# Kernel tuning notes

Measured on AMD Instinct MI355X. Metric: run time of the kernel, lower is better.

The kernel has to match this reference:

```python
import jax, jax.numpy as jnp
import numpy as np

DIM = 1024
HEADS = 16
N_SENTS = 64
N_ENTS = 16
BATCH = 32


def setup_inputs() -> dict:
    key = jax.random.key(0)
    ks = jax.random.split(key, 16)
    S, E, B, D = N_SENTS, N_ENTS, BATCH, DIM
    sc = 1.0 / np.sqrt(D)
    f32 = jnp.float32
    return {
        "entities": jax.random.normal(ks[0], (S * E, B, D), f32),
        "padding_mask": jnp.zeros((S * E, B), bool),
        "n_sents": S,
        # learned aggregation query, init uniform(-1, 1) as in the module
        "query": jax.random.uniform(ks[1], (1, 1, D), f32, -1.0, 1.0),
        # do_proj key/val Linear layers (torch Linear convention: y = x @ W.T + b)
        "Wk_lin": jax.random.normal(ks[2], (D, D), f32) * sc,
        "bk_lin": jnp.zeros((D,), f32),
        "Wv_lin": jax.random.normal(ks[3], (D, D), f32) * sc,
        "bv_lin": jnp.zeros((D,), f32),
        # MultiheadAttention in-projection (split q/k/v) and out-projection
        "Wq_in": jax.random.normal(ks[4], (D, D), f32) * sc,
        "bq_in": jnp.zeros((D,), f32),
        "Wk_in": jax.random.normal(ks[5], (D, D), f32) * sc,
        "bk_in": jnp.zeros((D,), f32),
        "Wv_in": jax.random.normal(ks[6], (D, D), f32) * sc,
        "bv_in": jnp.zeros((D,), f32),
        "Wo": jax.random.normal(ks[7], (D, D), f32) * sc,
        "bo": jnp.zeros((D,), f32),
    }


def reference(entities, padding_mask, n_sents, query,
              Wk_lin, bk_lin, Wv_lin, bv_lin,
              Wq_in, bq_in, Wk_in, bk_in, Wv_in, bv_in, Wo, bo):
    SE, B, D = entities.shape
    E = SE // n_sents
    H = HEADS
    hd = D // H

    # do_proj key/value linears
    keys = entities @ Wk_lin.T + bk_lin   # [SE, B, D]
    vals = entities @ Wv_lin.T + bv_lin   # [SE, B, D]

    # MHA in-projections. Query is a single learned vector shared across
    # sentences and batch, so project once: [H, hd], pre-scaled by 1/sqrt(hd).
    q = ((query[0, 0] @ Wq_in.T + bq_in).reshape(H, hd)) * (1.0 / np.sqrt(hd))
    # Honor the block-diagonal mask: query s only sees its n_ents key slice,
    # so reshape keys/vals to [S, E, B, H, hd] and never build [S, S*E] scores.
    k = (keys @ Wk_in.T + bk_in).reshape(n_sents, E, B, H, hd)
    v = (vals @ Wv_in.T + bv_in).reshape(n_sents, E, B, H, hd)

    scores = jnp.einsum('hd,sebhd->sbhe', q, k)            # [S, B, H, E]
    pm = padding_mask.reshape(n_sents, E, B).transpose(0, 2, 1)  # [S, B, E]
    scores = jnp.where(pm[:, :, None, :], -jnp.inf, scores)
    attn = jax.nn.softmax(scores, axis=-1)                 # [S, B, H, E]
    ctx = jnp.einsum('sbhe,sebhd->sbhd', attn, v).reshape(n_sents, B, D)
    return ctx @ Wo.T + bo                                  # [S, B, D]
```

## Files before the change

kernel.cpp:

```cpp
#include <hip/hip_runtime.h>
#include <hip/hip_bf16.h>

constexpr int kD  = 1024;
constexpr int kH  = 16;
constexpr int kHD = 64;
constexpr int kS  = 64;
constexpr int kE  = 16;
constexpr int kB  = 32;
constexpr int kSB = kS * kB;

typedef __attribute__((ext_vector_type(8))) short bfvec8;
typedef __attribute__((ext_vector_type(4))) float fvec4;

struct __align__(8)  bf4  { __hip_bfloat16 v[4]; };
struct __align__(16) bf8v { __hip_bfloat16 v[8]; };


__global__ __launch_bounds__(256) void k_rowdot(const float* __restrict__ Wmat,
                                                const float* __restrict__ vec,
                                                const float* __restrict__ bias,
                                                float scale, float* __restrict__ outv) {
  int j = blockIdx.x;
  int t = threadIdx.x;
  const float4* w4 = (const float4*)(Wmat + (size_t)j * kD);
  const float4* v4 = (const float4*)vec;
  float4 a = w4[t], b = v4[t];
  float acc = a.x * b.x + a.y * b.y + a.z * b.z + a.w * b.w;
  #pragma unroll
  for (int o = 32; o >= 1; o >>= 1) acc += __shfl_xor(acc, o);
  __shared__ float red[4];
  if ((t & 63) == 0) red[t >> 6] = acc;
  __syncthreads();
  if (t == 0) outv[j] = (red[0] + red[1] + red[2] + red[3] + bias[j]) * scale;
}

__global__ __launch_bounds__(256) void k_w(const float* __restrict__ qs,
                                           const float* __restrict__ Wk_in,
                                           float* __restrict__ wmat) {
  int tid = blockIdx.x * 256 + threadIdx.x;
  int h = tid >> 10, d = tid & (kD - 1);
  float acc = 0.f;
  #pragma unroll 8
  for (int j = 0; j < kHD; j++)
    acc = fmaf(qs[h * kHD + j], Wk_in[(size_t)(h * kHD + j) * kD + d], acc);
  wmat[(size_t)h * kD + d] = acc;
}

__global__ __launch_bounds__(256) void k_c(const float* __restrict__ wmat,
                                           const float* __restrict__ bk_lin,
                                           const float* __restrict__ qs,
                                           const float* __restrict__ bk_in,
                                           float* __restrict__ cvec) {
  int t = threadIdx.x;
  int h = t >> 4, l = t & 15;
  float acc = 0.f;
  for (int d = l; d < kD; d += 16) acc += wmat[h * kD + d] * bk_lin[d];
  for (int j = l; j < kHD; j += 16) acc += qs[h * kHD + j] * bk_in[h * kHD + j];
  #pragma unroll
  for (int o = 8; o >= 1; o >>= 1) acc += __shfl_xor(acc, o, 16);
  if (l == 0) cvec[h] = acc;
}

__global__ void k_transpose_cvt(const float* __restrict__ in,
                                __hip_bfloat16* __restrict__ out) {
  __shared__ float tile[32][33];
  int x = blockIdx.x * 32 + threadIdx.x;
  int y0 = blockIdx.y * 32;
  for (int i = threadIdx.y; i < 32; i += 8)
    tile[i][threadIdx.x] = in[(size_t)(y0 + i) * kD + x];
  __syncthreads();
  int xo = blockIdx.y * 32 + threadIdx.x;
  int yo0 = blockIdx.x * 32;
  for (int i = threadIdx.y; i < 32; i += 8)
    out[(size_t)(yo0 + i) * kD + xo] = __float2bfloat16(tile[threadIdx.x][i]);
}


__global__ __launch_bounds__(256) void k_attn_eagg(const float* __restrict__ ent,
                                                   const unsigned char* __restrict__ pmask,
                                                   const __hip_bfloat16* __restrict__ Ubf,
                                                   const float* __restrict__ cvec,
                                                   __hip_bfloat16* __restrict__ eagg) {
  __shared__ __hip_bfloat16 ent_s[kE][kD + 8];
  __shared__ float sred[4][kE][kH + 1];
  __shared__ __hip_bfloat16 attn_b[kH][32];
  int sb = blockIdx.x;
  int s = sb >> 5, b = sb & 31;
  int t = threadIdx.x, l = t & 63, w = t >> 6;
  int quad = l >> 4, lane16 = l & 15;

  const float* src = ent + (size_t)(s * kE) * kB * kD + (size_t)b * kD;
  #pragma unroll
  for (int it = 0; it < 8; it++) {
    int i = t + it * 256;
    int e = i >> 7, f = (i & 127) * 8;
    const float4* pp = (const float4*)(src + (size_t)e * kB * kD + f);
    float4 v0 = pp[0], v1 = pp[1];
    bf8v pk;
    pk.v[0] = __float2bfloat16(v0.x); pk.v[1] = __float2bfloat16(v0.y);
    pk.v[2] = __float2bfloat16(v0.z); pk.v[3] = __float2bfloat16(v0.w);
    pk.v[4] = __float2bfloat16(v1.x); pk.v[5] = __float2bfloat16(v1.y);
    pk.v[6] = __float2bfloat16(v1.z); pk.v[7] = __float2bfloat16(v1.w);
    *(bf8v*)&ent_s[e][f] = pk;
  }
  __syncthreads();

  fvec4 sacc = {};
  #pragma unroll
  for (int ks = 0; ks < 8; ks++) {
    int k0 = w * 256 + ks * 32 + quad * 8;
    bfvec8 a = *(const bfvec8*)&ent_s[lane16][k0];
    bfvec8 bb = *(const bfvec8*)&Ubf[(size_t)lane16 * kD + k0];
    sacc = __builtin_amdgcn_mfma_f32_16x16x32_bf16(a, bb, sacc, 0, 0, 0);
  }
  #pragma unroll
  for (int i = 0; i < 4; i++) sred[w][quad * 4 + i][lane16] = sacc[i];
  __syncthreads();

  {
    int h = t >> 4, e = t & 15;
    float sc = sred[0][e][h] + sred[1][e][h] + sred[2][e][h] + sred[3][e][h] + cvec[h];
    if (pmask[(size_t)(s * kE + e) * kB + b]) sc = -INFINITY;
    float m = sc;
    #pragma unroll
    for (int o = 8; o >= 1; o >>= 1) m = fmaxf(m, __shfl_xor(m, o, 16));
    float ex = __expf(sc - m);
    float sum = ex;
    #pragma unroll
    for (int o = 8; o >= 1; o >>= 1) sum += __shfl_xor(sum, o, 16);
    attn_b[h][e] = __float2bfloat16(ex / sum);
    attn_b[h][e + 16] = __float2bfloat16(0.f);
  }
  __syncthreads();

  bfvec8 bfrag = *(const bfvec8*)&attn_b[lane16][quad * 8];
  __hip_bfloat16* dst = eagg + (size_t)sb * (kH * kD);
  for (int tt = 0; tt < 16; tt++) {
    int dme = (w * 16 + tt) * 16 + lane16;
    bfvec8 afrag = {};
    if (quad < 2) {
      #pragma unroll
      for (int j = 0; j < 8; j++)
        afrag[j] = *(const short*)&ent_s[quad * 8 + j][dme];
    }
    fvec4 acc = {};
    acc = __builtin_amdgcn_mfma_f32_16x16x32_bf16(afrag, bfrag, acc, 0, 0, 0);
    int d0 = (w * 16 + tt) * 16 + quad * 4;
    bf4 o;
    o.v[0] = __float2bfloat16(acc[0]); o.v[1] = __float2bfloat16(acc[1]);
    o.v[2] = __float2bfloat16(acc[2]); o.v[3] = __float2bfloat16(acc[3]);
    *(bf4*)&dst[(size_t)lane16 * kD + d0] = o;
  }
}


__device__ __forceinline__ void stage_row(const __hip_bfloat16* g, __hip_bfloat16* s) {
  *(bf8v*)s = *(const bf8v*)g;
}
__device__ __forceinline__ void stage_row(const float* g, __hip_bfloat16* s) {
  const float4* p = (const float4*)g;
  float4 v0 = p[0], v1 = p[1];
  bf8v pk;
  pk.v[0] = __float2bfloat16(v0.x); pk.v[1] = __float2bfloat16(v0.y);
  pk.v[2] = __float2bfloat16(v0.z); pk.v[3] = __float2bfloat16(v0.w);
  pk.v[4] = __float2bfloat16(v1.x); pk.v[5] = __float2bfloat16(v1.y);
  pk.v[6] = __float2bfloat16(v1.z); pk.v[7] = __float2bfloat16(v1.w);
  *(bf8v*)s = pk;
}

template <int MODE, typename TA, typename TB, typename TC>
__global__ __launch_bounds__(256) void k_gemm_mfma(
    const TA* __restrict__ Abase, int lda, long aBatch,
    const TB* __restrict__ Bbase, int ldb, long bBatch,
    TC* __restrict__ Cbase, int ldc, long cBatch,
    const float* __restrict__ bias, long biasBatch, int Ksz) {
  const TA* Ag = Abase + (size_t)blockIdx.z * aBatch;
  const TB* Bg = Bbase + (size_t)blockIdx.z * bBatch;
  TC* Cg = Cbase + (size_t)blockIdx.z * cBatch;
  const float* biasp = bias ? bias + (size_t)blockIdx.z * biasBatch : nullptr;
  const int m0 = blockIdx.x * 64, n0 = blockIdx.y * 64;
  __shared__ __hip_bfloat16 As[64][72];
  __shared__ __hip_bfloat16 Bs[64][72];
  const int t = threadIdx.x;
  const int l = t & 63, w = t >> 6;
  const int quad = l >> 4, col = l & 15;
  fvec4 acc[4] = {};
  for (int k0 = 0; k0 < Ksz; k0 += 64) {
    #pragma unroll
    for (int c = t; c < 512; c += 256) {
      int row = c >> 3, kq = (c & 7) * 8;
      stage_row(Ag + (size_t)(m0 + row) * lda + k0 + kq, &As[row][kq]);
      stage_row(Bg + (size_t)(n0 + row) * ldb + k0 + kq, &Bs[row][kq]);
    }
    __syncthreads();
    #pragma unroll
    for (int ks = 0; ks < 64; ks += 32) {
      bfvec8 a = *(const bfvec8*)&As[w * 16 + col][ks + quad * 8];
      #pragma unroll
      for (int nt = 0; nt < 4; nt++) {
        bfvec8 b = *(const bfvec8*)&Bs[nt * 16 + col][ks + quad * 8];
        acc[nt] = __builtin_amdgcn_mfma_f32_16x16x32_bf16(a, b, acc[nt], 0, 0, 0);
      }
    }
    __syncthreads();
  }
  #pragma unroll
  for (int nt = 0; nt < 4; nt++) {
    int n = n0 + nt * 16 + col;
    float bv = biasp ? biasp[n] : 0.f;
    #pragma unroll
    for (int i = 0; i < 4; i++) {
      int r = m0 + w * 16 + quad * 4 + i;
      float v = acc[nt][i] + bv;
      if constexpr (MODE == 0) {
        ((float*)Cg)[(size_t)r * ldc + n] = v;
      } else {
        ((__hip_bfloat16*)Cg)[(size_t)r * ldc + n] = __float2bfloat16(v);
      }
    }
  }
}

extern "C" void kernel_launch(void* const* d_in, const int* in_sizes, int n_in,
                              void* d_out, int out_size, void* d_ws, size_t ws_size,
                              hipStream_t stream) {
  const float* ent            = (const float*)d_in[0];
  const unsigned char* pmask  = (const unsigned char*)d_in[1];
  const float* query          = (const float*)d_in[3];
  const float* Wk_lin         = (const float*)d_in[4];
  const float* bk_lin         = (const float*)d_in[5];
  const float* Wv_lin         = (const float*)d_in[6];
  const float* bv_lin         = (const float*)d_in[7];
  const float* Wq_in          = (const float*)d_in[8];
  const float* bq_in          = (const float*)d_in[9];
  const float* Wk_in          = (const float*)d_in[10];
  const float* bk_in          = (const float*)d_in[11];
  const float* Wv_in          = (const float*)d_in[12];
  const float* bv_in          = (const float*)d_in[13];
  const float* Wo             = (const float*)d_in[14];
  const float* bo             = (const float*)d_in[15];
  float* out = (float*)d_out;

  float* p = (float*)d_ws;
  float* qs   = p; p += 1024;
  float* wmat = p; p += 64 * kD;
  float* cvec = p; p += 256;
  float* cb   = p; p += kD;
  __hip_bfloat16* bp = (__hip_bfloat16*)p;
  __hip_bfloat16* TT   = bp; bp += (size_t)kD * kD;
  __hip_bfloat16* Ubf  = bp; bp += (size_t)64 * kD;
  __hip_bfloat16* Mmat = bp; bp += (size_t)kD * kD;
  __hip_bfloat16* ctx2 = bp; bp += (size_t)kSB * kD;
  __hip_bfloat16* eagg = bp;

  k_rowdot<<<kD, 256, 0, stream>>>(Wq_in, query, bq_in, 0.125f, qs);
  k_w<<<64, 256, 0, stream>>>(qs, Wk_in, wmat);
  k_c<<<1, 256, 0, stream>>>(wmat, bk_lin, qs, bk_in, cvec);
  k_rowdot<<<kD, 256, 0, stream>>>(Wv_in, bv_lin, bv_in, 1.0f, cb);
  k_transpose_cvt<<<dim3(32, 32), dim3(32, 8), 0, stream>>>(Wk_lin, TT);
  k_gemm_mfma<2><<<dim3(1, 16, 1), 256, 0, stream>>>(
      wmat, kD, 0L, TT, kD, 0L, Ubf, kD, 0L, (const float*)nullptr, 0L, kD);
  k_transpose_cvt<<<dim3(32, 32), dim3(32, 8), 0, stream>>>(Wv_lin, TT);
  k_gemm_mfma<2><<<dim3(16, 16, 1), 256, 0, stream>>>(
      Wv_in, kD, 0L, TT, kD, 0L, Mmat, kD, 0L, (const float*)nullptr, 0L, kD);

  k_attn_eagg<<<kSB, 256, 0, stream>>>(ent, pmask, Ubf, cvec, eagg);
  k_gemm_mfma<2><<<dim3(kSB / 64, 1, kH), 256, 0, stream>>>(
      eagg, kH * kD, (long)kD, Mmat, kD, (long)(kHD * kD),
      ctx2, kD, (long)kHD, cb, (long)kHD, kD);
  k_gemm_mfma<0><<<dim3(kSB / 64, kD / 64, 1), 256, 0, stream>>>(
      ctx2, kD, 0L, Wo, kD, 0L, out, kD, 0L, bo, 0L, kD);
}
```

Baseline: 375.1 us.

## Use 128x64 GEMM tiles, pre-convert Wo to bf16, stage eagg stores via LDS

Adds a GEMM variant where each wave computes a 32x64 tile, so the block covers 128x64. Each B fragment is reused across two A fragments, and three GEMMs switch to it. Wo is converted to bf16 once up front instead of being restaged from fp32 in every tile. The attention kernel writes its aggregated output to shared memory first, then stores it to global memory in coalesced 16-byte chunks. In exchange, the bigger tiles halve the grid size on some GEMMs and LDS use rises in the attention kernel, which may lower occupancy.

```diff
diff --git a/kernel.cpp b/kernel.cpp
--- a/kernel.cpp
+++ b/kernel.cpp
@@ -75,6 +75,16 @@
     out[(size_t)(yo0 + i) * kD + xo] = __float2bfloat16(tile[threadIdx.x][i]);
 }
 
+__global__ __launch_bounds__(256) void k_cvt(const float* __restrict__ in,
+                                             __hip_bfloat16* __restrict__ out) {
+  int i = (blockIdx.x * 256 + threadIdx.x) * 4;
+  float4 v = *(const float4*)(in + i);
+  bf4 o;
+  o.v[0] = __float2bfloat16(v.x); o.v[1] = __float2bfloat16(v.y);
+  o.v[2] = __float2bfloat16(v.z); o.v[3] = __float2bfloat16(v.w);
+  *(bf4*)(out + i) = o;
+}
+
 
 __global__ __launch_bounds__(256) void k_attn_eagg(const float* __restrict__ ent,
                                                    const unsigned char* __restrict__ pmask,
@@ -82,6 +92,7 @@
                                                    const float* __restrict__ cvec,
                                                    __hip_bfloat16* __restrict__ eagg) {
   __shared__ __hip_bfloat16 ent_s[kE][kD + 8];
+  __shared__ __hip_bfloat16 eagg_s[kH][kD + 8];
   __shared__ float sred[4][kE][kH + 1];
   __shared__ __hip_bfloat16 attn_b[kH][32];
   int sb = blockIdx.x;
@@ -134,7 +145,6 @@
   __syncthreads();
 
   bfvec8 bfrag = *(const bfvec8*)&attn_b[lane16][quad * 8];
-  __hip_bfloat16* dst = eagg + (size_t)sb * (kH * kD);
   for (int tt = 0; tt < 16; tt++) {
     int dme = (w * 16 + tt) * 16 + lane16;
     bfvec8 afrag = {};
@@ -149,7 +159,16 @@
     bf4 o;
     o.v[0] = __float2bfloat16(acc[0]); o.v[1] = __float2bfloat16(acc[1]);
     o.v[2] = __float2bfloat16(acc[2]); o.v[3] = __float2bfloat16(acc[3]);
-    *(bf4*)&dst[(size_t)lane16 * kD + d0] = o;
+    *(bf4*)&eagg_s[lane16][d0] = o;
+  }
+  __syncthreads();
+
+  __hip_bfloat16* dstg = eagg + (size_t)sb * (kH * kD);
+  #pragma unroll
+  for (int it = 0; it < 8; it++) {
+    int c = t + it * 256;
+    int h = c >> 7, dq = (c & 127) * 8;
+    *(bf8v*)(dstg + (size_t)h * kD + dq) = *(const bf8v*)&eagg_s[h][dq];
   }
 }
 
@@ -212,10 +231,67 @@
     for (int i = 0; i < 4; i++) {
       int r = m0 + w * 16 + quad * 4 + i;
       float v = acc[nt][i] + bv;
-      if constexpr (MODE == 0) {
-        ((float*)Cg)[(size_t)r * ldc + n] = v;
-      } else {
-        ((__hip_bfloat16*)Cg)[(size_t)r * ldc + n] = __float2bfloat16(v);
+      if constexpr (MODE == 0) ((float*)Cg)[(size_t)r * ldc + n] = v;
+      else ((__hip_bfloat16*)Cg)[(size_t)r * ldc + n] = __float2bfloat16(v);
+    }
+  }
+}
+
+
+template <int MODE, typename TA, typename TB, typename TC>
+__global__ __launch_bounds__(256) void k_gemm_mfma2(
+    const TA* __restrict__ Abase, int lda, long aBatch,
+    const TB* __restrict__ Bbase, int ldb, long bBatch,
+    TC* __restrict__ Cbase, int ldc, long cBatch,
+    const float* __restrict__ bias, long biasBatch, int Ksz) {
+  const TA* Ag = Abase + (size_t)blockIdx.z * aBatch;
+  const TB* Bg = Bbase + (size_t)blockIdx.z * bBatch;
+  TC* Cg = Cbase + (size_t)blockIdx.z * cBatch;
+  const float* biasp = bias ? bias + (size_t)blockIdx.z * biasBatch : nullptr;
+  const int m0 = blockIdx.x * 128, n0 = blockIdx.y * 64;
+  __shared__ __hip_bfloat16 As[128][72];
+  __shared__ __hip_bfloat16 Bs[64][72];
+  const int t = threadIdx.x;
+  const int l = t & 63, w = t >> 6;
+  const int quad = l >> 4, col = l & 15;
+  fvec4 acc[2][4] = {};
+  for (int k0 = 0; k0 < Ksz; k0 += 64) {
+    #pragma unroll
+    for (int c = t; c < 1024; c += 256) {
+      int row = c >> 3, kq = (c & 7) * 8;
+      stage_row(Ag + (size_t)(m0 + row) * lda + k0 + kq, &As[row][kq]);
+    }
+    #pragma unroll
+    for (int c = t; c < 512; c += 256) {
+      int row = c >> 3, kq = (c & 7) * 8;
+      stage_row(Bg + (size_t)(n0 + row) * ldb + k0 + kq, &Bs[row][kq]);
+    }
+    __syncthreads();
+    #pragma unroll
+    for (int ks = 0; ks < 64; ks += 32) {
+      bfvec8 a0 = *(const bfvec8*)&As[w * 32 + col][ks + quad * 8];
+      bfvec8 a1 = *(const bfvec8*)&As[w * 32 + 16 + col][ks + quad * 8];
+      #pragma unroll
+      for (int nt = 0; nt < 4; nt++) {
+        bfvec8 b = *(const bfvec8*)&Bs[nt * 16 + col][ks + quad * 8];
+        acc[0][nt] = __builtin_amdgcn_mfma_f32_16x16x32_bf16(a0, b, acc[0][nt], 0, 0, 0);
+        acc[1][nt] = __builtin_amdgcn_mfma_f32_16x16x32_bf16(a1, b, acc[1][nt], 0, 0, 0);
+      }
+    }
+    __syncthreads();
+  }
+  #pragma unroll
+  for (int nt = 0; nt < 4; nt++) {
+    int n = n0 + nt * 16 + col;
+    float bv = biasp ? biasp[n] : 0.f;
+    #pragma unroll
+    for (int mi = 0; mi < 2; mi++) {
+      #pragma unroll
+      for (int i = 0; i < 4; i++) {
+        int r = m0 + w * 32 + mi * 16 + quad * 4 + i;
+        float v = acc[mi][nt][i] + bv;
+        if constexpr (MODE == 0) ((float*)Cg)[(size_t)r * ldc + n] = v;
+        else ((__hip_bfloat16*)Cg)[(size_t)r * ldc + n] = __float2bfloat16(v);
       }
     }
   }
@@ -250,9 +326,11 @@
   __hip_bfloat16* TT   = bp; bp += (size_t)kD * kD;
   __hip_bfloat16* Ubf  = bp; bp += (size_t)64 * kD;
   __hip_bfloat16* Mmat = bp; bp += (size_t)kD * kD;
+  __hip_bfloat16* Wobf = bp; bp += (size_t)kD * kD;
   __hip_bfloat16* ctx2 = bp; bp += (size_t)kSB * kD;
   __hip_bfloat16* eagg = bp;
 
+  k_cvt<<<kD, 256, 0, stream>>>(Wo, Wobf);
   k_rowdot<<<kD, 256, 0, stream>>>(Wq_in, query, bq_in, 0.125f, qs);
   k_w<<<64, 256, 0, stream>>>(qs, Wk_in, wmat);
   k_c<<<1, 256, 0, stream>>>(wmat, bk_lin, qs, bk_in, cvec);
@@ -261,13 +339,13 @@
   k_gemm_mfma<2><<<dim3(1, 16, 1), 256, 0, stream>>>(
       wmat, kD, 0L, TT, kD, 0L, Ubf, kD, 0L, (const float*)nullptr, 0L, kD);
   k_transpose_cvt<<<dim3(32, 32), dim3(32, 8), 0, stream>>>(Wv_lin, TT);
-  k_gemm_mfma<2><<<dim3(16, 16, 1), 256, 0, stream>>>(
+  k_gemm_mfma2<2><<<dim3(8, 16, 1), 256, 0, stream>>>(
       Wv_in, kD, 0L, TT, kD, 0L, Mmat, kD, 0L, (const float*)nullptr, 0L, kD);
 
   k_attn_eagg<<<kSB, 256, 0, stream>>>(ent, pmask, Ubf, cvec, eagg);
-  k_gemm_mfma<2><<<dim3(kSB / 64, 1, kH), 256, 0, stream>>>(
+  k_gemm_mfma2<2><<<dim3(kSB / 128, 1, kH), 256, 0, stream>>>(
       eagg, kH * kD, (long)kD, Mmat, kD, (long)(kHD * kD),
       ctx2, kD, (long)kHD, cb, (long)kHD, kD);
-  k_gemm_mfma<0><<<dim3(kSB / 64, kD / 64, 1), 256, 0, stream>>>(
-      ctx2, kD, 0L, Wo, kD, 0L, out, kD, 0L, bo, 0L, kD);
-}
+  k_gemm_mfma2<0><<<dim3(kSB / 128, kD / 64, 1), 256, 0, stream>>>(
+      ctx2, kD, 0L, Wobf, kD, 0L, out, kD, 0L, bo, 0L, kD);
+}
```

Result: slower. 419.0 us (+11.7%).

## Fuse weight-precompute kernels and fold transposes into an NN GEMM loader

Applied to the files above, without the earlier changes.

Merges the two row-dot kernels into one launch and folds the cvec reduction into the wmat kernel using atomics. It drops the separate transpose-convert passes by adding an NN GEMM that transposes while staging into shared memory. It also pre-converts Wo to bf16 so the final GEMM stages bf16 instead of fp32. The aim is fewer launches and less weight-preprocessing traffic, at the cost of strided LDS writes in the new loader and atomic ordering in cvec.

```diff
diff --git a/kernel.cpp b/kernel.cpp
--- a/kernel.cpp
+++ b/kernel.cpp
@@ -16,13 +16,24 @@
 struct __align__(16) bf8v { __hip_bfloat16 v[8]; };
 
 
-__global__ __launch_bounds__(256) void k_rowdot(const float* __restrict__ Wmat,
-                                                const float* __restrict__ vec,
-                                                const float* __restrict__ bias,
-                                                float scale, float* __restrict__ outv) {
-  int j = blockIdx.x;
-  int t = threadIdx.x;
-  const float4* w4 = (const float4*)(Wmat + (size_t)j * kD);
+__global__ __launch_bounds__(256) void k_pre(const float* __restrict__ Wq_in,
+                                             const float* __restrict__ query,
+                                             const float* __restrict__ bq_in,
+                                             const float* __restrict__ Wv_in,
+                                             const float* __restrict__ bv_lin,
+                                             const float* __restrict__ bv_in,
+                                             float* __restrict__ qs,
+                                             float* __restrict__ cb,
+                                             float* __restrict__ cvec) {
+  int j = blockIdx.x, t = threadIdx.x;
+  if (j == 0 && t < 16) cvec[t] = 0.f;
+  const float *W, *vec, *bias;
+  float scale;
+  float* outp;
+  int row;
+  if (j < 1024) { W = Wq_in; vec = query;  bias = bq_in; scale = 0.125f; outp = qs; row = j; }
+  else          { W = Wv_in; vec = bv_lin; bias = bv_in; scale = 1.0f;   outp = cb; row = j - 1024; }
+  const float4* w4 = (const float4*)(W + (size_t)row * kD);
   const float4* v4 = (const float4*)vec;
   float4 a = w4[t], b = v4[t];
   float acc = a.x * b.x + a.y * b.y + a.z * b.z + a.w * b.w;
@@ -31,12 +42,15 @@
   __shared__ float red[4];
   if ((t & 63) == 0) red[t >> 6] = acc;
   __syncthreads();
-  if (t == 0) outv[j] = (red[0] + red[1] + red[2] + red[3] + bias[j]) * scale;
-}
-
-__global__ __launch_bounds__(256) void k_w(const float* __restrict__ qs,
-                                           const float* __restrict__ Wk_in,
-                                           float* __restrict__ wmat) {
+  if (t == 0) outp[row] = (red[0] + red[1] + red[2] + red[3] + bias[row]) * scale;
+}
+
+__global__ __launch_bounds__(256) void k_w2(const float* __restrict__ qs,
+                                            const float* __restrict__ Wk_in,
+                                            const float* __restrict__ bk_lin,
+                                            const float* __restrict__ bk_in,
+                                            float* __restrict__ wmat,
+                                            float* __restrict__ cvec) {
   int tid = blockIdx.x * 256 + threadIdx.x;
   int h = tid >> 10, d = tid & (kD - 1);
   float acc = 0.f;
@@ -44,35 +58,21 @@
   for (int j = 0; j < kHD; j++)
     acc = fmaf(qs[h * kHD + j], Wk_in[(size_t)(h * kHD + j) * kD + d], acc);
   wmat[(size_t)h * kD + d] = acc;
-}
-
-__global__ __launch_bounds__(256) void k_c(const float* __restrict__ wmat,
-                                           const float* __restrict__ bk_lin,
-                                           const float* __restrict__ qs,
-                                           const float* __restrict__ bk_in,
-                                           float* __restrict__ cvec) {
-  int t = threadIdx.x;
-  int h = t >> 4, l = t & 15;
-  float acc = 0.f;
-  for (int d = l; d < kD; d += 16) acc += wmat[h * kD + d] * bk_lin[d];
-  for (int j = l; j < kHD; j += 16) acc += qs[h * kHD + j] * bk_in[h * kHD + j];
-  #pragma unroll
-  for (int o = 8; o >= 1; o >>= 1) acc += __shfl_xor(acc, o, 16);
-  if (l == 0) cvec[h] = acc;
-}
-
-__global__ void k_transpose_cvt(const float* __restrict__ in,
-                                __hip_bfloat16* __restrict__ out) {
-  __shared__ float tile[32][33];
-  int x = blockIdx.x * 32 + threadIdx.x;
-  int y0 = blockIdx.y * 32;
-  for (int i = threadIdx.y; i < 32; i += 8)
-    tile[i][threadIdx.x] = in[(size_t)(y0 + i) * kD + x];
-  __syncthreads();
-  int xo = blockIdx.y * 32 + threadIdx.x;
-  int yo0 = blockIdx.x * 32;
-  for (int i = threadIdx.y; i < 32; i += 8)
-    out[(size_t)(yo0 + i) * kD + xo] = __float2bfloat16(tile[threadIdx.x][i]);
+  float val = acc * bk_lin[d];
+  if (d < kHD) val += qs[h * kHD + d] * bk_in[h * kHD + d];
+  #pragma unroll
+  for (int o = 32; o >= 1; o >>= 1) val += __shfl_xor(val, o);
+  if ((threadIdx.x & 63) == 0) atomicAdd(&cvec[h], val);
+}
+
+__global__ __launch_bounds__(256) void k_cvt(const float* __restrict__ in,
+                                             __hip_bfloat16* __restrict__ out) {
+  int i = (blockIdx.x * 256 + threadIdx.x) * 4;
+  float4 v = *(const float4*)(in + i);
+  bf4 o;
+  o.v[0] = __float2bfloat16(v.x); o.v[1] = __float2bfloat16(v.y);
+  o.v[2] = __float2bfloat16(v.z); o.v[3] = __float2bfloat16(v.w);
+  *(bf4*)(out + i) = o;
 }
 
 
@@ -167,6 +167,7 @@
   pk.v[6] = __float2bfloat16(v1.z); pk.v[7] = __float2bfloat16(v1.w);
   *(bf8v*)s = pk;
 }
+
 
 template <int MODE, typename TA, typename TB, typename TC>
 __global__ __launch_bounds__(256) void k_gemm_mfma(
@@ -212,11 +213,59 @@
     for (int i = 0; i < 4; i++) {
       int r = m0 + w * 16 + quad * 4 + i;
       float v = acc[nt][i] + bv;
-      if constexpr (MODE == 0) {
-        ((float*)Cg)[(size_t)r * ldc + n] = v;
-      } else {
-        ((__hip_bfloat16*)Cg)[(size_t)r * ldc + n] = __float2bfloat16(v);
+      if constexpr (MODE == 0) ((float*)Cg)[(size_t)r * ldc + n] = v;
+      else ((__hip_bfloat16*)Cg)[(size_t)r * ldc + n] = __float2bfloat16(v);
+    }
+  }
+}
+
+
+__global__ __launch_bounds__(256) void k_gemm_nn(
+    const float* __restrict__ Ag, int lda,
+    const float* __restrict__ Bg, int ldb,
+    __hip_bfloat16* __restrict__ Cg, int ldc, int Ksz) {
+  const int m0 = blockIdx.x * 64, n0 = blockIdx.y * 64;
+  __shared__ __hip_bfloat16 As[64][72];
+  __shared__ __hip_bfloat16 Bs[64][72];
+  const int t = threadIdx.x;
+  const int l = t & 63, w = t >> 6;
+  const int quad = l >> 4, col = l & 15;
+  fvec4 acc[4] = {};
+  for (int k0 = 0; k0 < Ksz; k0 += 64) {
+    #pragma unroll
+    for (int c = t; c < 512; c += 256) {
+      int row = c >> 3, kq = (c & 7) * 8;
+      stage_row(Ag + (size_t)(m0 + row) * lda + k0 + kq, &As[row][kq]);
+      const float4* pb = (const float4*)(Bg + (size_t)(k0 + row) * ldb + n0 + kq);
+      float4 b0 = pb[0], b1 = pb[1];
+      Bs[kq + 0][row] = __float2bfloat16(b0.x);
+      Bs[kq + 1][row] = __float2bfloat16(b0.y);
+      Bs[kq + 2][row] = __float2bfloat16(b0.z);
+      Bs[kq + 3][row] = __float2bfloat16(b0.w);
+      Bs[kq + 4][row] = __float2bfloat16(b1.x);
+      Bs[kq + 5][row] = __float2bfloat16(b1.y);
+      Bs[kq + 6][row] = __float2bfloat16(b1.z);
+      Bs[kq + 7][row] = __float2bfloat16(b1.w);
+    }
+    __syncthreads();
+    #pragma unroll
+    for (int ks = 0; ks < 64; ks += 32) {
+      bfvec8 a = *(const bfvec8*)&As[w * 16 + col][ks + quad * 8];
+      #pragma unroll
+      for (int nt = 0; nt < 4; nt++) {
+        bfvec8 b = *(const bfvec8*)&Bs[nt * 16 + col][ks + quad * 8];
+        acc[nt] = __builtin_amdgcn_mfma_f32_16x16x32_bf16(a, b, acc[nt], 0, 0, 0);
       }
+    }
+    __syncthreads();
+  }
+  #pragma unroll
+  for (int nt = 0; nt < 4; nt++) {
+    int n = n0 + nt * 16 + col;
+    #pragma unroll
+    for (int i = 0; i < 4; i++) {
+      int r = m0 + w * 16 + quad * 4 + i;
+      Cg[(size_t)r * ldc + n] = __float2bfloat16(acc[nt][i]);
     }
   }
 }
@@ -247,27 +296,22 @@
   float* cvec = p; p += 256;
   float* cb   = p; p += kD;
   __hip_bfloat16* bp = (__hip_bfloat16*)p;
-  __hip_bfloat16* TT   = bp; bp += (size_t)kD * kD;
   __hip_bfloat16* Ubf  = bp; bp += (size_t)64 * kD;
   __hip_bfloat16* Mmat = bp; bp += (size_t)kD * kD;
+  __hip_bfloat16* Wobf = bp; bp += (size_t)kD * kD;
   __hip_bfloat16* ctx2 = bp; bp += (size_t)kSB * kD;
   __hip_bfloat16* eagg = bp;
 
-  k_rowdot<<<kD, 256, 0, stream>>>(Wq_in, query, bq_in, 0.125f, qs);
-  k_w<<<64, 256, 0, stream>>>(qs, Wk_in, wmat);
-  k_c<<<1, 256, 0, stream>>>(wmat, bk_lin, qs, bk_in, cvec);
-  k_rowdot<<<kD, 256, 0, stream>>>(Wv_in, bv_lin, bv_in, 1.0f, cb);
-  k_transpose_cvt<<<dim3(32, 32), dim3(32, 8), 0, stream>>>(Wk_lin, TT);
-  k_gemm_mfma<2><<<dim3(1, 16, 1), 256, 0, stream>>>(
-      wmat, kD, 0L, TT, kD, 0L, Ubf, kD, 0L, (const float*)nullptr, 0L, kD);
-  k_transpose_cvt<<<dim3(32, 32), dim3(32, 8), 0, stream>>>(Wv_lin, TT);
-  k_gemm_mfma<2><<<dim3(16, 16, 1), 256, 0, stream>>>(
-      Wv_in, kD, 0L, TT, kD, 0L, Mmat, kD, 0L, (const float*)nullptr, 0L, kD);
+  k_pre<<<2048, 256, 0, stream>>>(Wq_in, query, bq_in, Wv_in, bv_lin, bv_in, qs, cb, cvec);
+  k_w2<<<64, 256, 0, stream>>>(qs, Wk_in, bk_lin, bk_in, wmat, cvec);
+  k_cvt<<<1024, 256, 0, stream>>>(Wo, Wobf);
+  k_gemm_nn<<<dim3(1, 16, 1), 256, 0, stream>>>(wmat, kD, Wk_lin, kD, Ubf, kD, kD);
+  k_gemm_nn<<<dim3(16, 16, 1), 256, 0, stream>>>(Wv_in, kD, Wv_lin, kD, Mmat, kD, kD);
 
   k_attn_eagg<<<kSB, 256, 0, stream>>>(ent, pmask, Ubf, cvec, eagg);
   k_gemm_mfma<2><<<dim3(kSB / 64, 1, kH), 256, 0, stream>>>(
       eagg, kH * kD, (long)kD, Mmat, kD, (long)(kHD * kD),
       ctx2, kD, (long)kHD, cb, (long)kHD, kD);
   k_gemm_mfma<0><<<dim3(kSB / 64, kD / 64, 1), 256, 0, stream>>>(
-      ctx2, kD, 0L, Wo, kD, 0L, out, kD, 0L, bo, 0L, kD);
-}
+      ctx2, kD, 0L, Wobf, kD, 0L, out, kD, 0L, bo, 0L, kD);
+}
```

Result: faster. 355.4 us (-5.2%).
